# Optimization experiments

Measured on AMD Instinct MI355X. Metric: run time of the kernel, lower is better.

The kernel has to match this reference:

```python
import jax, jax.numpy as jnp
import numpy as np

IN = 128; HID = 128; OUT = 128; HEADS = 3; T1 = 0.2; T2 = 0.2
B = 512; L = 32; V = 100000; NMETA = 5


def _corr_full(s, t):
    # s, t: (B, L, E, N). Full cross-correlation along last axis.
    # Matches F.conv1d(hs, ht, groups=BLE, padding=N-1): out[k] = sum_m s[k+m-(N-1)] * t[m]
    N = s.shape[-1]
    sp = jnp.pad(s, ((0, 0), (0, 0), (0, 0), (N - 1, N - 1)))
    out = jnp.stack([(sp[..., k:k + N] * t).sum(-1) for k in range(2 * N - 1)], axis=-1)
    return jnp.swapaxes(out, -1, -2)  # (B, L, 2N-1, E)


def _node_att(h, Wt, Ws, Wc):
    # h: (B, L, P, E); Wt/Ws/Wc: (HEADS, E, HID)
    Bh, Lh, P, E = h.shape
    H = h.reshape(Bh * Lh, P, E)
    hi = jnp.einsum('ne,heo->hno', H[:, 0], Wt)                 # target-node projection
    logits = jnp.einsum('npe,heo,hno->hnp', H, Ws, hi) / T1     # (heads, BL, P)
    alpha = jax.nn.softmax(logits, axis=-1)                     # softmax over path positions
    Z = jnp.einsum('hnp,npe,heo->no', alpha, H, Wc) / HEADS     # mean over heads
    return Z.reshape(Bh, Lh, -1)


def _forward(emb_user, emb_item, emb_attr1, emb_attr2, emb_attr3, Wt, Ws, Wc,
             pw1, pb1, pw2, fw1, fb1, fw2, fb2,
             UI, IU, UIUI, IUIU, UIAI1, IAIU1, UIAI2, IAIU2, UIAI3, IAIU3):
    src = emb_user[UI[:, 0, 0]]
    tgt = emb_item[IU[:, 0, 0]]
    ui = jnp.stack([emb_user[UI[..., 0]], emb_item[UI[..., 1]]], axis=3)
    iu = jnp.stack([emb_item[IU[..., 0]], emb_user[IU[..., 1]]], axis=3)

    def p4(tabs, idx):
        return jnp.stack([tabs[k][idx[..., k]] for k in range(4)], axis=3)

    uiui = p4([emb_user, emb_item, emb_user, emb_item], UIUI)
    iuiu = p4([emb_item, emb_user, emb_item, emb_user], IUIU)
    uiai1 = p4([emb_user, emb_item, emb_attr1, emb_item], UIAI1)
    iaiu1 = p4([emb_item, emb_attr1, emb_item, emb_user], IAIU1)
    uiai2 = p4([emb_user, emb_item, emb_attr2, emb_item], UIAI2)
    iaiu2 = p4([emb_item, emb_attr2, emb_item, emb_user], IAIU2)
    uiai3 = p4([emb_user, emb_item, emb_attr3, emb_item], UIAI3)
    iaiu3 = p4([emb_item, emb_attr3, emb_item, emb_user], IAIU3)

    user_feats = [ui, uiui, uiai1, uiai2, uiai3]
    item_feats = [iu, iuiu, iaiu1, iaiu2, iaiu3]
    Hs = [_node_att(_corr_full(uf, itf), Wt[m], Ws[m], Wc[m])
          for m, (uf, itf) in enumerate(zip(user_feats, item_feats))]
    Z = jnp.stack(Hs, 1)                        # (B, 5, L, HID)
    z = Z.reshape(Z.shape[0], -1, HID)          # (B, 5L, HID)
    w = jnp.tanh(z @ pw1 + pb1) @ pw2 / T2      # (B, 5L, 1)
    beta = jax.nn.softmax(w, axis=1)
    path_out = (beta * z).sum(1)                # (B, HID)
    x = jnp.concatenate([src, tgt, path_out], axis=1)
    x = jax.nn.relu(x @ fw1 + fb1)              # dropout in eval mode -> identity
    return jax.nn.sigmoid(x @ fw2 + fb2)        # (B, 1)


def setup_inputs() -> dict:
    key = jax.random.key(0)
    ks = jax.random.split(key, 24)

    def idx(k, n):
        return jax.random.randint(k, (B, L, n), 0, V, dtype=jnp.int32)

    d = {
        'UI': idx(ks[0], 2), 'IU': idx(ks[1], 2),
        'UIUI': idx(ks[2], 4), 'IUIU': idx(ks[3], 4),
        'UIAI1': idx(ks[4], 4), 'IAIU1': idx(ks[5], 4),
        'UIAI2': idx(ks[6], 4), 'IAIU2': idx(ks[7], 4),
        'UIAI3': idx(ks[8], 4), 'IAIU3': idx(ks[9], 4),
    }

    def emb(k):
        t = jax.random.normal(k, (V + 1, IN), jnp.float32) * 0.05
        return t.at[0].set(0.0)  # padding_idx=0

    d['emb_user'] = emb(ks[10]); d['emb_item'] = emb(ks[11])
    d['emb_attr1'] = emb(ks[12]); d['emb_attr2'] = emb(ks[13]); d['emb_attr3'] = emb(ks[14])
    s = (2.0 / (IN + HID)) ** 0.5  # xavier scale
    d['Wt'] = jax.random.normal(ks[15], (NMETA, HEADS, IN, HID), jnp.float32) * s
    d['Ws'] = jax.random.normal(ks[16], (NMETA, HEADS, IN, HID), jnp.float32) * s
    d['Wc'] = jax.random.normal(ks[17], (NMETA, HEADS, IN, HID), jnp.float32) * s
    d['pw1'] = jax.random.normal(ks[18], (HID, HID), jnp.float32) * s
    d['pb1'] = jnp.zeros((HID,), jnp.float32)
    d['pw2'] = jax.random.normal(ks[19], (HID, 1), jnp.float32) * s
    d['fw1'] = jax.random.normal(ks[20], (3 * HID, OUT), jnp.float32) * 0.02
    d['fb1'] = jnp.zeros((OUT,), jnp.float32)
    d['fw2'] = jax.random.normal(ks[21], (OUT, 1), jnp.float32) * 0.02
    d['fb2'] = jnp.zeros((1,), jnp.float32)
    return d


def reference(UI, IU, UIUI, IUIU, UIAI1, IAIU1, UIAI2, IAIU2, UIAI3, IAIU3,
              emb_user, emb_item, emb_attr1, emb_attr2, emb_attr3,
              Wt, Ws, Wc, pw1, pb1, pw2, fw1, fb1, fw2, fb2):
    return _forward(emb_user, emb_item, emb_attr1, emb_attr2, emb_attr3, Wt, Ws, Wc,
                    pw1, pb1, pw2, fw1, fb1, fw2, fb2,
                    UI, IU, UIUI, IUIU, UIAI1, IAIU1, UIAI2, IAIU2, UIAI3, IAIU3)
```

## Files before the change

### kernel.cpp

```cpp
#include <hip/hip_runtime.h>
#include <hip/hip_bf16.h>
#include <cstdint>
#include <cstddef>


typedef __hip_bfloat16 bf16;
typedef __attribute__((ext_vector_type(8))) short  bfrag;
typedef __attribute__((ext_vector_type(4))) float  ffrag;

#define NNODES 16384

__device__ __forceinline__ float bflo(uint32_t u) { return __uint_as_float(u << 16); }
__device__ __forceinline__ float bfhi(uint32_t u) { return __uint_as_float(u & 0xffff0000u); }

__global__ __launch_bounds__(256) void build_BmatT(
    const float* __restrict__ Ws, const float* __restrict__ Wt,
    bf16* __restrict__ BmT)
{
  int mh = blockIdx.x >> 4;
  int g  = blockIdx.x & 15;
  int m = mh / 3, h = mh % 3;
  const float* ws = Ws + (size_t)mh * 16384;
  const float* wt = Wt + (size_t)mh * 16384;
  int tid = threadIdx.x;
  int e = tid & 127, half = tid >> 7;
  __shared__ float wtl[2][128];
  for (int ep0 = g * 8; ep0 < g * 8 + 8; ep0 += 2) {
    int ep = ep0 + half;
    wtl[half][e] = wt[ep * 128 + e];
    __syncthreads();
    float acc = 0.f;
    #pragma unroll 4
    for (int o = 0; o < 128; ++o) acc += ws[e * 128 + o] * wtl[half][o];
    BmT[((size_t)(m * 384 + h * 128 + e)) * 128 + ep] = __float2bfloat16(acc);
    __syncthreads();
  }
}

__global__ __launch_bounds__(256) void conv_WcT(
    const float* __restrict__ Wc, bf16* __restrict__ WcT)
{
  int idx = blockIdx.x * 256 + threadIdx.x;
  int he = idx % 384, mo = idx / 384;
  int m = mo >> 7, o = mo & 127;
  WcT[idx] = __float2bfloat16(Wc[((size_t)m * 384 + he) * 128 + o]);
}

__global__ __launch_bounds__(256) void conv_pw1T(
    const float* __restrict__ pw1, bf16* __restrict__ pw1T)
{
  int idx = blockIdx.x * 256 + threadIdx.x;
  int o = idx >> 7, k = idx & 127;
  pw1T[idx] = __float2bfloat16(pw1[(size_t)k * 128 + o]);
}

template <int P>
__device__ __forceinline__ void metapath_body(
    char* smem,
    const float* __restrict__ Tu0, const float* __restrict__ Tu1,
    const float* __restrict__ Tu2, const float* __restrict__ Tu3,
    const float* __restrict__ Tt0, const float* __restrict__ Tt1,
    const float* __restrict__ Tt2, const float* __restrict__ Tt3,
    const int* __restrict__ idxU, const int* __restrict__ idxT,
    const bf16* __restrict__ BmT,
    const bf16* __restrict__ WcT,
    bf16* __restrict__ Zall, int m, int tile)
{
  constexpr int PP = 2 * P - 1;
  constexpr int NS = PP * 136;
  constexpr int NPAIR = 3 * PP;
  bf16*  Hs    = (bf16*)smem;
  bf16*  Ss    = (bf16*)(smem + 16 * NS * 2);
  float* lg    = (float*)(smem + 16 * NS * 2 + 16 * 392 * 2);
  float* alpha = lg + 16 * 3 * 8;

  int tid = threadIdx.x;
  int lane = tid & 63, wid = tid >> 6;
  int l15 = lane & 15, l4 = lane >> 4;
  int n0 = tile * 16;

  {
    const float* TU[4] = {Tu0, Tu1, Tu2, Tu3};
    const float* TT[4] = {Tt0, Tt1, Tt2, Tt3};
    int e = tid & 127;
    float su[4][P], st[4][P];
    #pragma unroll
    for (int g = 0; g < 4; ++g) {
      int n = n0 + g * 4 + (tid >> 7);
      #pragma unroll
      for (int p = 0; p < P; ++p) {
        su[g][p] = TU[p][(size_t)idxU[n * P + p] * 128 + e];
        st[g][p] = TT[p][(size_t)idxT[n * P + p] * 128 + e];
      }
    }
    #pragma unroll
    for (int g = 0; g < 4; ++g) {
      int ln = g * 4 + (tid >> 7);
      bf16* Hn = &Hs[ln * NS + e];
      #pragma unroll
      for (int k = 0; k < PP; ++k) {
        float acc = 0.f;
        #pragma unroll
        for (int i = 0; i < P; ++i) {
          int j = k + i - (P - 1);
          if (j >= 0 && j < P) acc += su[g][j] * st[g][i];
        }
        Hn[k * 136] = __float2bfloat16(acc);
      }
    }
  }
  __syncthreads();

  {
    bfrag a[4];
    #pragma unroll
    for (int kk = 0; kk < 4; ++kk)
      a[kk] = *(const bfrag*)&Hs[l15 * NS + kk * 32 + 8 * l4];
    #pragma unroll
    for (int f = 0; f < 3; ++f) {
      int col = wid * 48 + f * 16 + l15;
      ffrag acc = {0.f, 0.f, 0.f, 0.f};
      #pragma unroll
      for (int kk = 0; kk < 4; ++kk) {
        bfrag b = *(const bfrag*)&BmT[(size_t)col * 128 + kk * 32 + 8 * l4];
        acc = __builtin_amdgcn_mfma_f32_16x16x32_bf16(a[kk], b, acc, 0, 0, 0);
      }
      #pragma unroll
      for (int r = 0; r < 4; ++r) {
        int node = 4 * l4 + r;
        Ss[node * 392 + col] = __float2bfloat16(acc[r]);
      }
    }
  }
  __syncthreads();

  {
    int node = tid >> 5, q = tid & 31;
    if (q < NPAIR) {
      int h = q / PP, p = q - h * PP;
      const uint32_t* hrow = (const uint32_t*)&Hs[node * NS + p * 136];
      const uint32_t* srow = (const uint32_t*)&Ss[node * 392 + h * 128];
      float acc = 0.f;
      #pragma unroll 8
      for (int i = 0; i < 64; ++i) {
        uint32_t hv = hrow[i], sv = srow[i];
        acc += bflo(hv) * bflo(sv) + bfhi(hv) * bfhi(sv);
      }
      lg[(node * 3 + h) * 8 + p] = acc * 5.0f;
    }
  }
  __syncthreads();

  if (tid < 48) {
    float mx = -1e30f;
    #pragma unroll
    for (int p = 0; p < PP; ++p) mx = fmaxf(mx, lg[tid * 8 + p]);
    float s = 0.f, ev[8];
    #pragma unroll
    for (int p = 0; p < PP; ++p) { ev[p] = expf(lg[tid * 8 + p] - mx); s += ev[p]; }
    float inv = 1.0f / s;
    #pragma unroll
    for (int p = 0; p < PP; ++p) alpha[tid * 8 + p] = ev[p] * inv;
  }
  __syncthreads();

  {
    int node = tid >> 5, q = tid & 31;
    #pragma unroll
    for (int c = 0; c < 6; ++c) {
      int o2 = q * 6 + c;
      int h = o2 >> 6, e = (o2 & 63) * 2;
      float a0 = 0.f, a1 = 0.f;
      #pragma unroll
      for (int p = 0; p < PP; ++p) {
        float al = alpha[(node * 3 + h) * 8 + p];
        uint32_t hv = *(const uint32_t*)&Hs[node * NS + p * 136 + e];
        a0 += al * bflo(hv);
        a1 += al * bfhi(hv);
      }
      Ss[node * 392 + h * 128 + e]     = __float2bfloat16(a0);
      Ss[node * 392 + h * 128 + e + 1] = __float2bfloat16(a1);
    }
  }
  __syncthreads();

  {
    bfrag a[12];
    #pragma unroll
    for (int kk = 0; kk < 12; ++kk)
      a[kk] = *(const bfrag*)&Ss[l15 * 392 + kk * 32 + 8 * l4];
    int col = wid * 16 + l15;
    ffrag acc = {0.f, 0.f, 0.f, 0.f};
    #pragma unroll
    for (int kk = 0; kk < 12; ++kk) {
      bfrag b = *(const bfrag*)&WcT[(size_t)col * 384 + kk * 32 + 8 * l4];
      acc = __builtin_amdgcn_mfma_f32_16x16x32_bf16(a[kk], b, acc, 0, 0, 0);
    }
    #pragma unroll
    for (int r = 0; r < 4; ++r) {
      int gn = n0 + 4 * l4 + r;
      int crow = (((gn >> 5) * 5 + m) << 5) + (gn & 31);
      Zall[(size_t)crow * 128 + col] = __float2bfloat16(acc[r] * (1.0f / 3.0f));
    }
  }
}

__global__ __launch_bounds__(512) void fused_all(
    const float* __restrict__ emb_user, const float* __restrict__ emb_item,
    const float* __restrict__ emb_a1, const float* __restrict__ emb_a2,
    const float* __restrict__ emb_a3,
    const int* __restrict__ UI,    const int* __restrict__ IU,
    const int* __restrict__ UIUI,  const int* __restrict__ IUIU,
    const int* __restrict__ UIAI1, const int* __restrict__ IAIU1,
    const int* __restrict__ UIAI2, const int* __restrict__ IAIU2,
    const int* __restrict__ UIAI3, const int* __restrict__ IAIU3,
    const bf16* __restrict__ BmT, const bf16* __restrict__ WcT,
    bf16* __restrict__ Zall)
{
  extern __shared__ char smem[];
  int bid = blockIdx.x;
  int m = bid >> 10, tile = bid & 1023;
  if (m == 0) {
    metapath_body<2>(smem, emb_user, emb_item, nullptr, nullptr,
                     emb_item, emb_user, nullptr, nullptr,
                     UI, IU, BmT, WcT, Zall, 0, tile);
  } else {
    const float* u2 = (m == 1) ? emb_user : (m == 2) ? emb_a1
                    : (m == 3) ? emb_a2 : emb_a3;
    const int* iu_ = (m == 1) ? UIUI : (m == 2) ? UIAI1
                   : (m == 3) ? UIAI2 : UIAI3;
    const int* it_ = (m == 1) ? IUIU : (m == 2) ? IAIU1
                   : (m == 3) ? IAIU2 : IAIU3;
    metapath_body<4>(smem, emb_user, emb_item, u2, emb_item,
                     emb_item, u2, emb_item, emb_user,
                     iu_, it_,
                     BmT + (size_t)m * 49152, WcT + (size_t)m * 49152,
                     Zall, m, tile);
  }
}

__global__ __launch_bounds__(512) void fused_tail(
    const bf16* __restrict__ Zall,
    const bf16* __restrict__ pw1T,
    const float* __restrict__ pb1, const float* __restrict__ pw2,
    const int* __restrict__ UI, const int* __restrict__ IU,
    const float* __restrict__ emb_user, const float* __restrict__ emb_item,
    const float* __restrict__ fw1, const float* __restrict__ fb1,
    const float* __restrict__ fw2, const float* __restrict__ fb2,
    float* __restrict__ out)
{
  __shared__ bf16 Zs[160 * 136];
  __shared__ float wrow[160];
  __shared__ float ph[4][128];
  __shared__ float xs[384];
  __shared__ float sred[16];
  __shared__ float yred[2];

  int b = blockIdx.x, tid = threadIdx.x;
  int lane = tid & 63, wid = tid >> 6;
  int l15 = lane & 15, l4 = lane >> 4;

  {
    const float4* src = (const float4*)(Zall + (size_t)b * 160 * 128);
    float4 v[5];
    #pragma unroll
    for (int i = 0; i < 5; ++i) v[i] = src[i * 512 + tid];
    #pragma unroll
    for (int i = 0; i < 5; ++i) {
      int idx = i * 512 + tid;
      int row = idx >> 4, c8 = idx & 15;
      *(float4*)&Zs[row * 136 + c8 * 8] = v[i];
    }
  }
  __syncthreads();

  for (int rf = wid; rf < 10; rf += 8) {
    bfrag a[4];
    #pragma unroll
    for (int kk = 0; kk < 4; ++kk)
      a[kk] = *(const bfrag*)&Zs[(rf * 16 + l15) * 136 + kk * 32 + 8 * l4];
    float part[4] = {0.f, 0.f, 0.f, 0.f};
    #pragma unroll
    for (int f = 0; f < 8; ++f) {
      int col = f * 16 + l15;
      ffrag acc = {0.f, 0.f, 0.f, 0.f};
      #pragma unroll
      for (int kk = 0; kk < 4; ++kk) {
        bfrag bv = *(const bfrag*)&pw1T[(size_t)col * 128 + kk * 32 + 8 * l4];
        acc = __builtin_amdgcn_mfma_f32_16x16x32_bf16(a[kk], bv, acc, 0, 0, 0);
      }
      float bias = pb1[col], w2 = pw2[col];
      #pragma unroll
      for (int r = 0; r < 4; ++r) part[r] += tanhf(acc[r] + bias) * w2;
    }
    #pragma unroll
    for (int d = 1; d < 16; d <<= 1) {
      #pragma unroll
      for (int r = 0; r < 4; ++r) part[r] += __shfl_xor(part[r], d);
    }
    if (l15 == 0) {
      #pragma unroll
      for (int r = 0; r < 4; ++r)
        wrow[rf * 16 + 4 * l4 + r] = part[r] * 5.0f;
    }
  }
  __syncthreads();

  {
    float v = (tid < 160) ? wrow[tid] : -1e30f;
    #pragma unroll
    for (int off = 32; off; off >>= 1) v = fmaxf(v, __shfl_xor(v, off));
    if (lane == 0) sred[wid] = v;
    __syncthreads();
    if (tid < 64) {
      float mval = (lane < 8) ? sred[lane] : -1e30f;
      #pragma unroll
      for (int off = 4; off; off >>= 1) mval = fmaxf(mval, __shfl_xor(mval, off));
      if (lane == 0) sred[8] = mval;
    }
    __syncthreads();
    float mx = sred[8];
    float ev = (tid < 160) ? expf(wrow[tid] - mx) : 0.f;
    float s = ev;
    #pragma unroll
    for (int off = 32; off; off >>= 1) s += __shfl_xor(s, off);
    if (lane == 0) sred[wid] = s;
    __syncthreads();
    if (tid < 64) {
      float sval = (lane < 8) ? sred[lane] : 0.f;
      #pragma unroll
      for (int off = 4; off; off >>= 1) sval += __shfl_xor(sval, off);
      if (lane == 0) sred[9] = sval;
    }
    __syncthreads();
    if (tid < 160) wrow[tid] = ev / sred[9];
  }
  __syncthreads();

  {
    int e = tid & 127, q = tid >> 7;
    float acc = 0.f;
    #pragma unroll 4
    for (int j = q * 40; j < q * 40 + 40; ++j)
      acc += wrow[j] * __bfloat162float(Zs[j * 136 + e]);
    ph[q][e] = acc;
  }
  __syncthreads();

  {
    int su = UI[b * 64];
    int ti = IU[b * 64];
    if (tid < 128) {
      xs[256 + tid] = ph[0][tid] + ph[1][tid] + ph[2][tid] + ph[3][tid];
    } else if (tid < 256) {
      xs[tid - 128] = emb_user[(size_t)su * 128 + (tid - 128)];
    } else if (tid < 384) {
      xs[tid - 128] = emb_item[(size_t)ti * 128 + (tid - 256)];
    }
  }
  __syncthreads();

  {
    int o = tid & 127, q = tid >> 7;
    float acc = 0.f;
    #pragma unroll 4
    for (int i = q * 96; i < q * 96 + 96; ++i)
      acc += xs[i] * fw1[(size_t)i * 128 + o];
    __syncthreads();
    ph[q][o] = acc;
  }
  __syncthreads();
  if (tid < 128) {
    float y = fmaxf(ph[0][tid] + ph[1][tid] + ph[2][tid] + ph[3][tid] + fb1[tid],
                    0.0f) * fw2[tid];
    #pragma unroll
    for (int off = 32; off; off >>= 1) y += __shfl_down(y, off);
    if ((tid & 63) == 0) yred[tid >> 6] = y;
  }
  __syncthreads();
  if (tid == 0) {
    float s = yred[0] + yred[1] + fb2[0];
    out[b] = 1.0f / (1.0f + expf(-s));
  }
}

extern "C" void kernel_launch(void* const* d_in, const int* in_sizes, int n_in,
                              void* d_out, int out_size, void* d_ws, size_t ws_size,
                              hipStream_t stream)
{
  const int* UI    = (const int*)d_in[0];
  const int* IU    = (const int*)d_in[1];
  const int* UIUI  = (const int*)d_in[2];
  const int* IUIU  = (const int*)d_in[3];
  const int* UIAI1 = (const int*)d_in[4];
  const int* IAIU1 = (const int*)d_in[5];
  const int* UIAI2 = (const int*)d_in[6];
  const int* IAIU2 = (const int*)d_in[7];
  const int* UIAI3 = (const int*)d_in[8];
  const int* IAIU3 = (const int*)d_in[9];
  const float* emb_user = (const float*)d_in[10];
  const float* emb_item = (const float*)d_in[11];
  const float* emb_a1   = (const float*)d_in[12];
  const float* emb_a2   = (const float*)d_in[13];
  const float* emb_a3   = (const float*)d_in[14];
  const float* Wt  = (const float*)d_in[15];
  const float* Ws  = (const float*)d_in[16];
  const float* Wc  = (const float*)d_in[17];
  const float* pw1 = (const float*)d_in[18];
  const float* pb1 = (const float*)d_in[19];
  const float* pw2 = (const float*)d_in[20];
  const float* fw1 = (const float*)d_in[21];
  const float* fb1 = (const float*)d_in[22];
  const float* fw2 = (const float*)d_in[23];
  const float* fb2 = (const float*)d_in[24];
  float* out = (float*)d_out;

  char* wsb = (char*)d_ws;
  bf16*  BmT  = (bf16*)wsb;
  bf16*  WcT  = (bf16*)(wsb + 491520);
  bf16*  pw1T = (bf16*)(wsb + 983040);
  bf16*  Zall = (bf16*)(wsb + 1015808);

  build_BmatT<<<240, 256, 0, stream>>>(Ws, Wt, BmT);
  conv_WcT<<<960, 256, 0, stream>>>(Wc, WcT);
  conv_pw1T<<<64, 256, 0, stream>>>(pw1, pw1T);

  fused_all<<<5120, 512, 46080, stream>>>(
      emb_user, emb_item, emb_a1, emb_a2, emb_a3,
      UI, IU, UIUI, IUIU, UIAI1, IAIU1, UIAI2, IAIU2, UIAI3, IAIU3,
      BmT, WcT, Zall);

  fused_tail<<<512, 512, 0, stream>>>(Zall, pw1T, pb1, pw2,
                                      UI, IU, emb_user, emb_item,
                                      fw1, fb1, fw2, fb2, out);
}
```

Baseline: 216.3 us.

## Halve metapath tile to 8 nodes and move attention logits/softmax/weighted sum to MFMA

The fused metapath kernel now processes 8 nodes per 256-thread block instead of 16 per 512 threads, doubling the grid and allowing more blocks per CU. The scalar logits dot products, the separate softmax pass and the alpha-weighted sum over path positions are replaced with MFMA instructions and wave-shuffle softmax, using an extra transposed H buffer so alpha×H can be done as a matrix product. This removes two barriers and scalar LDS loops. In exchange, the 16-row MFMA tiles are half-used (rows padded or clamped) and weights are reloaded per smaller tile. expf is also swapped for __expf.

```diff
diff --git a/kernel.cpp b/kernel.cpp
--- a/kernel.cpp
+++ b/kernel.cpp
@@ -12,6 +12,13 @@
 
 __device__ __forceinline__ float bflo(uint32_t u) { return __uint_as_float(u << 16); }
 __device__ __forceinline__ float bfhi(uint32_t u) { return __uint_as_float(u & 0xffff0000u); }
+__device__ __forceinline__ uint16_t f2bfu(float x) {
+  bf16 h = __float2bfloat16(x);
+  return *(uint16_t*)&h;
+}
+__device__ __forceinline__ uint32_t pk2(float lo, float hi) {
+  return (uint32_t)f2bfu(lo) | ((uint32_t)f2bfu(hi) << 16);
+}
 
 __global__ __launch_bounds__(256) void build_BmatT(
     const float* __restrict__ Ws, const float* __restrict__ Wt,
@@ -68,25 +75,25 @@
 {
   constexpr int PP = 2 * P - 1;
   constexpr int NS = PP * 136;
-  constexpr int NPAIR = 3 * PP;
-  bf16*  Hs    = (bf16*)smem;
-  bf16*  Ss    = (bf16*)(smem + 16 * NS * 2);
-  float* lg    = (float*)(smem + 16 * NS * 2 + 16 * 392 * 2);
-  float* alpha = lg + 16 * 3 * 8;
+  bf16* Hs = (bf16*)smem;
+  bf16* Ht = Hs + 8 * NS;
+  bf16* Ss = Ht + 8 * 1024;
+  bf16* Al = Ss + 8 * 392;
 
   int tid = threadIdx.x;
   int lane = tid & 63, wid = tid >> 6;
   int l15 = lane & 15, l4 = lane >> 4;
-  int n0 = tile * 16;
-
-  {
+  int n0 = tile * 8;
+
+  {
+    for (int i = tid; i < 8 * 96 / 2; i += 256) ((uint32_t*)Al)[i] = 0;
     const float* TU[4] = {Tu0, Tu1, Tu2, Tu3};
     const float* TT[4] = {Tt0, Tt1, Tt2, Tt3};
     int e = tid & 127;
     float su[4][P], st[4][P];
     #pragma unroll
     for (int g = 0; g < 4; ++g) {
-      int n = n0 + g * 4 + (tid >> 7);
+      int n = n0 + g * 2 + (tid >> 7);
       #pragma unroll
       for (int p = 0; p < P; ++p) {
         su[g][p] = TU[p][(size_t)idxU[n * P + p] * 128 + e];
@@ -95,30 +102,42 @@
     }
     #pragma unroll
     for (int g = 0; g < 4; ++g) {
-      int ln = g * 4 + (tid >> 7);
-      bf16* Hn = &Hs[ln * NS + e];
+      int ln = g * 2 + (tid >> 7);
+      float acc[PP];
       #pragma unroll
       for (int k = 0; k < PP; ++k) {
-        float acc = 0.f;
+        float a = 0.f;
         #pragma unroll
         for (int i = 0; i < P; ++i) {
           int j = k + i - (P - 1);
-          if (j >= 0 && j < P) acc += su[g][j] * st[g][i];
+          if (j >= 0 && j < P) a += su[g][j] * st[g][i];
         }
-        Hn[k * 136] = __float2bfloat16(acc);
-      }
+        acc[k] = a;
+        Hs[ln * NS + k * 136 + e] = __float2bfloat16(a);
+      }
+      int4 w;
+      w.x = pk2(acc[0], acc[1]);
+      w.y = pk2(acc[2], (PP > 3) ? acc[3] : 0.f);
+      if (PP > 3) {
+        w.z = pk2(acc[4], acc[5]);
+        w.w = pk2(acc[6], 0.f);
+      } else {
+        w.z = 0; w.w = 0;
+      }
+      *(int4*)&Ht[(ln * 128 + e) * 8] = w;
     }
   }
   __syncthreads();
 
   {
     bfrag a[4];
+    int nrow = (l15 < 7) ? l15 : 7;
     #pragma unroll
     for (int kk = 0; kk < 4; ++kk)
-      a[kk] = *(const bfrag*)&Hs[l15 * NS + kk * 32 + 8 * l4];
-    #pragma unroll
-    for (int f = 0; f < 3; ++f) {
-      int col = wid * 48 + f * 16 + l15;
+      a[kk] = *(const bfrag*)&Hs[nrow * NS + kk * 32 + 8 * l4];
+    #pragma unroll
+    for (int f = 0; f < 6; ++f) {
+      int col = wid * 96 + f * 16 + l15;
       ffrag acc = {0.f, 0.f, 0.f, 0.f};
       #pragma unroll
       for (int kk = 0; kk < 4; ++kk) {
@@ -128,84 +147,99 @@
       #pragma unroll
       for (int r = 0; r < 4; ++r) {
         int node = 4 * l4 + r;
-        Ss[node * 392 + col] = __float2bfloat16(acc[r]);
-      }
-    }
-  }
-  __syncthreads();
-
-  {
-    int node = tid >> 5, q = tid & 31;
-    if (q < NPAIR) {
-      int h = q / PP, p = q - h * PP;
-      const uint32_t* hrow = (const uint32_t*)&Hs[node * NS + p * 136];
-      const uint32_t* srow = (const uint32_t*)&Ss[node * 392 + h * 128];
-      float acc = 0.f;
-      #pragma unroll 8
-      for (int i = 0; i < 64; ++i) {
-        uint32_t hv = hrow[i], sv = srow[i];
-        acc += bflo(hv) * bflo(sv) + bfhi(hv) * bfhi(sv);
-      }
-      lg[(node * 3 + h) * 8 + p] = acc * 5.0f;
-    }
-  }
-  __syncthreads();
-
-  if (tid < 48) {
-    float mx = -1e30f;
-    #pragma unroll
-    for (int p = 0; p < PP; ++p) mx = fmaxf(mx, lg[tid * 8 + p]);
-    float s = 0.f, ev[8];
-    #pragma unroll
-    for (int p = 0; p < PP; ++p) { ev[p] = expf(lg[tid * 8 + p] - mx); s += ev[p]; }
-    float inv = 1.0f / s;
-    #pragma unroll
-    for (int p = 0; p < PP; ++p) alpha[tid * 8 + p] = ev[p] * inv;
-  }
-  __syncthreads();
-
-  {
-    int node = tid >> 5, q = tid & 31;
-    #pragma unroll
-    for (int c = 0; c < 6; ++c) {
-      int o2 = q * 6 + c;
-      int h = o2 >> 6, e = (o2 & 63) * 2;
-      float a0 = 0.f, a1 = 0.f;
-      #pragma unroll
-      for (int p = 0; p < PP; ++p) {
-        float al = alpha[(node * 3 + h) * 8 + p];
-        uint32_t hv = *(const uint32_t*)&Hs[node * NS + p * 136 + e];
-        a0 += al * bflo(hv);
-        a1 += al * bfhi(hv);
-      }
-      Ss[node * 392 + h * 128 + e]     = __float2bfloat16(a0);
-      Ss[node * 392 + h * 128 + e + 1] = __float2bfloat16(a1);
+        if (node < 8) Ss[node * 392 + col] = __float2bfloat16(acc[r]);
+      }
+    }
+  }
+  __syncthreads();
+
+  {
+    int hrow = (l15 < 2) ? l15 : 2;
+    int prow = (l15 < PP - 1) ? l15 : (PP - 1);
+    #pragma unroll
+    for (int nn = 0; nn < 2; ++nn) {
+      int node = wid * 2 + nn;
+      const bf16* SsN = Ss + node * 392;
+      const bf16* HsN = Hs + node * NS;
+      ffrag lacc = {0.f, 0.f, 0.f, 0.f};
+      #pragma unroll
+      for (int kk = 0; kk < 4; ++kk) {
+        bfrag a = *(const bfrag*)&SsN[hrow * 128 + kk * 32 + 8 * l4];
+        bfrag b = *(const bfrag*)&HsN[prow * 136 + kk * 32 + 8 * l4];
+        lacc = __builtin_amdgcn_mfma_f32_16x16x32_bf16(a, b, lacc, 0, 0, 0);
+      }
+      bool val = (l4 == 0) && (l15 < PP);
+      float l0 = val ? lacc[0] * 5.0f : -1e30f;
+      float l1 = val ? lacc[1] * 5.0f : -1e30f;
+      float l2 = val ? lacc[2] * 5.0f : -1e30f;
+      float m0 = l0, m1 = l1, m2 = l2;
+      #pragma unroll
+      for (int d = 1; d < 8; d <<= 1) {
+        m0 = fmaxf(m0, __shfl_xor(m0, d));
+        m1 = fmaxf(m1, __shfl_xor(m1, d));
+        m2 = fmaxf(m2, __shfl_xor(m2, d));
+      }
+      float e0 = val ? __expf(l0 - m0) : 0.f;
+      float e1 = val ? __expf(l1 - m1) : 0.f;
+      float e2 = val ? __expf(l2 - m2) : 0.f;
+      float s0 = e0, s1 = e1, s2 = e2;
+      #pragma unroll
+      for (int d = 1; d < 8; d <<= 1) {
+        s0 += __shfl_xor(s0, d);
+        s1 += __shfl_xor(s1, d);
+        s2 += __shfl_xor(s2, d);
+      }
+      if (val) {
+        Al[node * 96 +      l15] = __float2bfloat16(e0 / s0);
+        Al[node * 96 + 32 + l15] = __float2bfloat16(e1 / s1);
+        Al[node * 96 + 64 + l15] = __float2bfloat16(e2 / s2);
+      }
+      bfrag aa = *(const bfrag*)&Al[node * 96 + hrow * 32 + 8 * l4];
+      #pragma unroll
+      for (int f = 0; f < 8; ++f) {
+        bfrag bb = *(const bfrag*)&Ht[(node * 128 + f * 16 + l15) * 8];
+        ffrag hb = {0.f, 0.f, 0.f, 0.f};
+        hb = __builtin_amdgcn_mfma_f32_16x16x32_bf16(aa, bb, hb, 0, 0, 0);
+        if (l4 == 0) {
+          #pragma unroll
+          for (int r = 0; r < 3; ++r)
+            Ss[node * 392 + r * 128 + f * 16 + l15] = __float2bfloat16(hb[r]);
+        }
+      }
     }
   }
   __syncthreads();
 
   {
     bfrag a[12];
+    int nrow = (l15 < 7) ? l15 : 7;
     #pragma unroll
     for (int kk = 0; kk < 12; ++kk)
-      a[kk] = *(const bfrag*)&Ss[l15 * 392 + kk * 32 + 8 * l4];
-    int col = wid * 16 + l15;
-    ffrag acc = {0.f, 0.f, 0.f, 0.f};
-    #pragma unroll
-    for (int kk = 0; kk < 12; ++kk) {
-      bfrag b = *(const bfrag*)&WcT[(size_t)col * 384 + kk * 32 + 8 * l4];
-      acc = __builtin_amdgcn_mfma_f32_16x16x32_bf16(a[kk], b, acc, 0, 0, 0);
-    }
-    #pragma unroll
-    for (int r = 0; r < 4; ++r) {
-      int gn = n0 + 4 * l4 + r;
-      int crow = (((gn >> 5) * 5 + m) << 5) + (gn & 31);
-      Zall[(size_t)crow * 128 + col] = __float2bfloat16(acc[r] * (1.0f / 3.0f));
-    }
-  }
-}
-
-__global__ __launch_bounds__(512) void fused_all(
+      a[kk] = *(const bfrag*)&Ss[nrow * 392 + kk * 32 + 8 * l4];
+    #pragma unroll
+    for (int f = 0; f < 2; ++f) {
+      int col = wid * 32 + f * 16 + l15;
+      ffrag acc = {0.f, 0.f, 0.f, 0.f};
+      #pragma unroll
+      for (int kk = 0; kk < 12; ++kk) {
+        bfrag b = *(const bfrag*)&WcT[(size_t)col * 384 + kk * 32 + 8 * l4];
+        acc = __builtin_amdgcn_mfma_f32_16x16x32_bf16(a[kk], b, acc, 0, 0, 0);
+      }
+      #pragma unroll
+      for (int r = 0; r < 4; ++r) {
+        int node = 4 * l4 + r;
+        if (node < 8) {
+          int gn = n0 + node;
+          int crow = (((gn >> 5) * 5 + m) << 5) + (gn & 31);
+          Zall[(size_t)crow * 128 + col] =
+              __float2bfloat16(acc[r] * (1.0f / 3.0f));
+        }
+      }
+    }
+  }
+}
+
+__global__ __launch_bounds__(256, 4) void fused_all(
     const float* __restrict__ emb_user, const float* __restrict__ emb_item,
     const float* __restrict__ emb_a1, const float* __restrict__ emb_a2,
     const float* __restrict__ emb_a3,
@@ -219,7 +253,7 @@
 {
   extern __shared__ char smem[];
   int bid = blockIdx.x;
-  int m = bid >> 10, tile = bid & 1023;
+  int m = bid >> 11, tile = bid & 2047;
   if (m == 0) {
     metapath_body<2>(smem, emb_user, emb_item, nullptr, nullptr,
                      emb_item, emb_user, nullptr, nullptr,
@@ -320,7 +354,7 @@
     }
     __syncthreads();
     float mx = sred[8];
-    float ev = (tid < 160) ? expf(wrow[tid] - mx) : 0.f;
+    float ev = (tid < 160) ? __expf(wrow[tid] - mx) : 0.f;
     float s = ev;
     #pragma unroll
     for (int off = 32; off; off >>= 1) s += __shfl_xor(s, off);
@@ -425,7 +459,7 @@
   conv_WcT<<<960, 256, 0, stream>>>(Wc, WcT);
   conv_pw1T<<<64, 256, 0, stream>>>(pw1, pw1T);
 
-  fused_all<<<5120, 512, 46080, stream>>>(
+  fused_all<<<10240, 256, 39424, stream>>>(
       emb_user, emb_item, emb_a1, emb_a2, emb_a3,
       UI, IU, UIUI, IUIU, UIAI1, IAIU1, UIAI2, IAIU2, UIAI3, IAIU3,
       BmT, WcT, Zall);
```

After: 309.1 us. 1.43x slower.

## Fuse logit, softmax and weighted-sum stages with wave shuffles in metapath body

Applied to the files above, without the earlier changes.

Merges the per-node logit dot products, softmax over path positions, and the alpha-weighted sum into one phase. Softmax values move between lanes by wave shuffles instead of through shared memory, which removes two block barriers and the lg/alpha buffers and shrinks dynamic shared memory. The dot-product loop uses 64-bit loads, a per-head rotated start index to spread LDS bank access, and four partial accumulators. Outputs are written as packed bf16 pairs, and expf becomes __expf in both softmaxes, which slightly lowers precision.

```diff
diff --git a/kernel.cpp b/kernel.cpp
--- a/kernel.cpp
+++ b/kernel.cpp
@@ -12,6 +12,13 @@
 
 __device__ __forceinline__ float bflo(uint32_t u) { return __uint_as_float(u << 16); }
 __device__ __forceinline__ float bfhi(uint32_t u) { return __uint_as_float(u & 0xffff0000u); }
+__device__ __forceinline__ uint16_t f2bfu(float x) {
+  bf16 h = __float2bfloat16(x);
+  return *(uint16_t*)&h;
+}
+__device__ __forceinline__ uint32_t pk2(float lo, float hi) {
+  return (uint32_t)f2bfu(lo) | ((uint32_t)f2bfu(hi) << 16);
+}
 
 __global__ __launch_bounds__(256) void build_BmatT(
     const float* __restrict__ Ws, const float* __restrict__ Wt,
@@ -69,10 +76,8 @@
   constexpr int PP = 2 * P - 1;
   constexpr int NS = PP * 136;
   constexpr int NPAIR = 3 * PP;
-  bf16*  Hs    = (bf16*)smem;
-  bf16*  Ss    = (bf16*)(smem + 16 * NS * 2);
-  float* lg    = (float*)(smem + 16 * NS * 2 + 16 * 392 * 2);
-  float* alpha = lg + 16 * 3 * 8;
+  bf16* Hs = (bf16*)smem;
+  bf16* Ss = Hs + 16 * NS;
 
   int tid = threadIdx.x;
   int lane = tid & 63, wid = tid >> 6;
@@ -136,50 +141,54 @@
 
   {
     int node = tid >> 5, q = tid & 31;
+    int h = q / PP, p = q - h * PP;
+    float alpha_mine = 0.f;
+    float lg = -1e30f;
     if (q < NPAIR) {
-      int h = q / PP, p = q - h * PP;
-      const uint32_t* hrow = (const uint32_t*)&Hs[node * NS + p * 136];
-      const uint32_t* srow = (const uint32_t*)&Ss[node * 392 + h * 128];
-      float acc = 0.f;
-      #pragma unroll 8
-      for (int i = 0; i < 64; ++i) {
-        uint32_t hv = hrow[i], sv = srow[i];
-        acc += bflo(hv) * bflo(sv) + bfhi(hv) * bfhi(sv);
-      }
-      lg[(node * 3 + h) * 8 + p] = acc * 5.0f;
-    }
-  }
-  __syncthreads();
-
-  if (tid < 48) {
-    float mx = -1e30f;
-    #pragma unroll
-    for (int p = 0; p < PP; ++p) mx = fmaxf(mx, lg[tid * 8 + p]);
-    float s = 0.f, ev[8];
-    #pragma unroll
-    for (int p = 0; p < PP; ++p) { ev[p] = expf(lg[tid * 8 + p] - mx); s += ev[p]; }
-    float inv = 1.0f / s;
-    #pragma unroll
-    for (int p = 0; p < PP; ++p) alpha[tid * 8 + p] = ev[p] * inv;
-  }
-  __syncthreads();
-
-  {
-    int node = tid >> 5, q = tid & 31;
+      const uint2* hrow = (const uint2*)&Hs[node * NS + p * 136];
+      const uint2* srow = (const uint2*)&Ss[node * 392 + h * 128];
+      float acc[4] = {0.f, 0.f, 0.f, 0.f};
+      int rot = h * 10;
+      #pragma unroll
+      for (int ii = 0; ii < 32; ++ii) {
+        int iu = (ii + rot) & 31;
+        uint2 hv = hrow[iu], sv = srow[iu];
+        float t = bflo(hv.x) * bflo(sv.x) + bfhi(hv.x) * bfhi(sv.x)
+                + bflo(hv.y) * bflo(sv.y) + bfhi(hv.y) * bfhi(sv.y);
+        acc[ii & 3] += t;
+      }
+      lg = (acc[0] + acc[1] + acc[2] + acc[3]) * 5.0f;
+    }
+    int base = (lane & 32) + h * PP;
+    float mx = lg;
+    #pragma unroll
+    for (int d = 1; d < PP; ++d) {
+      int pd = p + d; if (pd >= PP) pd -= PP;
+      mx = fmaxf(mx, __shfl(lg, base + pd, 64));
+    }
+    float ex = __expf(lg - mx);
+    float sm = ex;
+    #pragma unroll
+    for (int d = 1; d < PP; ++d) {
+      int pd = p + d; if (pd >= PP) pd -= PP;
+      sm += __shfl(ex, base + pd, 64);
+    }
+    alpha_mine = ex / sm;
+
+    int hb = lane & 32;
     #pragma unroll
     for (int c = 0; c < 6; ++c) {
       int o2 = q * 6 + c;
-      int h = o2 >> 6, e = (o2 & 63) * 2;
+      int h2 = o2 >> 6, e2 = (o2 & 63) * 2;
       float a0 = 0.f, a1 = 0.f;
       #pragma unroll
-      for (int p = 0; p < PP; ++p) {
-        float al = alpha[(node * 3 + h) * 8 + p];
-        uint32_t hv = *(const uint32_t*)&Hs[node * NS + p * 136 + e];
+      for (int pp = 0; pp < PP; ++pp) {
+        float al = __shfl(alpha_mine, hb + h2 * PP + pp, 64);
+        uint32_t hv = *(const uint32_t*)&Hs[node * NS + pp * 136 + e2];
         a0 += al * bflo(hv);
         a1 += al * bfhi(hv);
       }
-      Ss[node * 392 + h * 128 + e]     = __float2bfloat16(a0);
-      Ss[node * 392 + h * 128 + e + 1] = __float2bfloat16(a1);
+      *(uint32_t*)&Ss[node * 392 + h2 * 128 + e2] = pk2(a0, a1);
     }
   }
   __syncthreads();
@@ -320,7 +329,7 @@
     }
     __syncthreads();
     float mx = sred[8];
-    float ev = (tid < 160) ? expf(wrow[tid] - mx) : 0.f;
+    float ev = (tid < 160) ? __expf(wrow[tid] - mx) : 0.f;
     float s = ev;
     #pragma unroll
     for (int off = 32; off; off >>= 1) s += __shfl_xor(s, off);
@@ -425,7 +434,7 @@
   conv_WcT<<<960, 256, 0, stream>>>(Wc, WcT);
   conv_pw1T<<<64, 256, 0, stream>>>(pw1, pw1T);
 
-  fused_all<<<5120, 512, 46080, stream>>>(
+  fused_all<<<5120, 512, 43008, stream>>>(
       emb_user, emb_item, emb_a1, emb_a2, emb_a3,
       UI, IU, UIUI, IUIU, UIAI1, IAIU1, UIAI2, IAIU2, UIAI3, IAIU3,
       BmT, WcT, Zall);
```

Result: slower. 241.6 us (+11.7%).
